# Performance work log

Measured on AMD Instinct MI355X. Metric: run time of the kernel, lower is better.

Reference implementation:

```python
import jax, jax.numpy as jnp
import numpy as np

N, V, D, H, E = 16384, 17, 128, 256, 32
LN_EPS = 1e-5


def setup_inputs() -> dict:
    key = jax.random.key(0)
    ks = jax.random.split(key, 16)
    s = lambda *sh: 1.0 / np.sqrt(sh[0])
    inp = {
        "h": jax.random.normal(ks[0], (N, V, D), dtype=jnp.float32),
        "xy": jax.random.normal(ks[1], (N, V, 2), dtype=jnp.float32),
        "joint_mask": jax.random.randint(ks[2], (N, V), 0, 2).astype(bool),
        "edge_index": jax.random.randint(ks[3], (E, 2), 0, V).astype(jnp.int64),
        # edge MLP: Linear(2D+2 -> H), ReLU, Linear(H -> D)
        "ew1": jax.random.normal(ks[4], (2 * D + 2, H), dtype=jnp.float32) * s(2 * D + 2),
        "eb1": jnp.zeros((H,), dtype=jnp.float32),
        "ew2": jax.random.normal(ks[5], (H, D), dtype=jnp.float32) * s(H),
        "eb2": jnp.zeros((D,), dtype=jnp.float32),
        # node MLP: Linear(2D -> H), ReLU, Linear(H -> D)
        "nw1": jax.random.normal(ks[6], (2 * D, H), dtype=jnp.float32) * s(2 * D),
        "nb1": jnp.zeros((H,), dtype=jnp.float32),
        "nw2": jax.random.normal(ks[7], (H, D), dtype=jnp.float32) * s(H),
        "nb2": jnp.zeros((D,), dtype=jnp.float32),
        # LayerNorm(D)
        "gamma": jnp.ones((D,), dtype=jnp.float32),
        "beta": jnp.zeros((D,), dtype=jnp.float32),
    }
    return inp


def reference(h, xy, joint_mask, edge_index, ew1, eb1, ew2, eb2,
              nw1, nb1, nw2, nb2, gamma, beta):
    dst = edge_index[:, 0]  # [E]
    src = edge_index[:, 1]  # [E]
    mask_f = joint_mask.astype(h.dtype)  # [N,V]

    target = h[:, dst, :]                  # [N,E,D]
    source = h[:, src, :]                  # [N,E,D]
    rel = xy[:, src, :] - xy[:, dst, :]    # [N,E,2]
    edge_valid = (joint_mask[:, dst] & joint_mask[:, src]).astype(h.dtype)  # [N,E]

    msg_in = jnp.concatenate([target, source, rel], axis=-1)  # [N,E,2D+2]
    msg = jax.nn.relu(msg_in @ ew1 + eb1) @ ew2 + eb2          # [N,E,D]
    msg = msg * edge_valid[..., None]

    agg = jnp.zeros_like(h).at[:, dst, :].add(msg)                           # [N,V,D]
    denom = jnp.zeros((h.shape[0], h.shape[1], 1), h.dtype).at[:, dst, :].add(
        edge_valid[..., None])                                               # [N,V,1]
    agg = agg / jnp.maximum(denom, 1.0)

    delta = jax.nn.relu(jnp.concatenate([h, agg], axis=-1) @ nw1 + nb1) @ nw2 + nb2
    has_neighbors = (denom > 0).astype(h.dtype)
    x = h + delta * has_neighbors

    mu = jnp.mean(x, axis=-1, keepdims=True)
    var = jnp.mean(jnp.square(x - mu), axis=-1, keepdims=True)
    out = (x - mu) / jnp.sqrt(var + LN_EPS) * gamma + beta
    return out * mask_f[..., None]
```

## Files before the change

kernel.cpp:

```cpp
#include <hip/hip_runtime.h>

typedef _Float16 half8 __attribute__((ext_vector_type(8)));
typedef _Float16 half4v __attribute__((ext_vector_type(4)));
typedef float f32x4 __attribute__((ext_vector_type(4)));
typedef unsigned int u32;

#define LDH 136

__global__ void prep_weights(const float* __restrict__ ew1,
                             const float* __restrict__ ew2,
                             const float* __restrict__ nw1,
                             const float* __restrict__ nw2,
                             _Float16* __restrict__ wz) {
  int o = blockIdx.x * 256 + threadIdx.x;
  if (o < 65536) {
    int s = o >> 12, r = o & 4095;
    int gs = r >> 9, lane = (r >> 3) & 63, j = r & 7;
    int k = ((s & 1) * 4 + (gs >> 1)) * 32 + (lane >> 4) * 8 + j;
    int n = (s >> 1) * 32 + (gs & 1) * 16 + (lane & 15);
    wz[o] = (_Float16)ew1[k * 256 + n];
  } else if (o < 98304) {
    int o2 = o - 65536;
    int nc = o2 >> 12, r = o2 & 4095;
    int nt2 = r >> 9, lane = (r >> 3) & 63, j = r & 7;
    int k = nc * 32 + (lane >> 4) * 8 + j;
    int n = nt2 * 16 + (lane & 15);
    wz[o] = (_Float16)ew2[k * 128 + n];
  } else if (o < 163840) {
    int o2 = o - 98304;
    int s = o2 >> 12, r = o2 & 4095;
    int gs = r >> 9, lane = (r >> 3) & 63, j = r & 7;
    int k = ((s & 1) * 4 + (gs >> 1)) * 32 + (lane >> 4) * 8 + j;
    int n = (s >> 1) * 32 + (gs & 1) * 16 + (lane & 15);
    wz[o] = (_Float16)nw1[k * 256 + n];
  } else if (o < 196608) {
    int o2 = o - 163840;
    int nc = o2 >> 12, r = o2 & 4095;
    int nt2 = r >> 9, lane = (r >> 3) & 63, j = r & 7;
    int k = nc * 32 + (lane >> 4) * 8 + j;
    int n = nt2 * 16 + (lane & 15);
    wz[o] = (_Float16)nw2[k * 128 + n];
  }
}

__global__ __launch_bounds__(256, 2)
void fused_graph_layer(const float* __restrict__ h, const float* __restrict__ xy,
                       const int* __restrict__ jmask, const int* __restrict__ eidx,
                       const float* __restrict__ ew1,
                       const float* __restrict__ eb1, const float* __restrict__ eb2,
                       const float* __restrict__ nb1, const float* __restrict__ nb2,
                       const float* __restrict__ gamma, const float* __restrict__ beta,
                       const _Float16* __restrict__ wz,
                       float* __restrict__ out) {
  __shared__ _Float16 sh_h16[68 * LDH];
  __shared__ _Float16 sh_agg16[68 * LDH];
  __shared__ char uni[36864] __attribute__((aligned(16)));
  __shared__ float sh_rel[256];
  __shared__ float sh_valid[128];
  __shared__ float sh_dn[80];
  __shared__ float sh_hasn[68], sh_maskf[68];
  __shared__ int   sh_edge[64];

  const int tid  = threadIdx.x;
  const int wave = tid >> 6;
  const int lane = tid & 63;
  const int ln   = lane & 15;
  const int quad = lane >> 4;
  const int n0   = blockIdx.x * 4;
  const size_t hbase = (size_t)n0 * 2176;
  const f32x4 vzero = {0.f, 0.f, 0.f, 0.f};

  _Float16* ws = (_Float16*)(uni + wave * 9216);

  const _Float16* w1img  = wz;
  const _Float16* w2img  = wz + 65536;
  const _Float16* nw1img = wz + 98304;
  const _Float16* nw2img = wz + 163840;
  const float* w1r0 = ew1 + 256 * 256;
  const float* w1r1 = ew1 + 257 * 256;

  if (tid < 64) sh_edge[tid] = eidx[tid];
  if (tid < 68) sh_maskf[tid] = (float)jmask[n0 * 17 + tid];
  for (int i = tid; i < 2176; i += 256) {
    const float4 hv = ((const float4*)(h + hbase))[i];
    int q = i << 2;
    int gv = q >> 7, d = q & 127;
    half4v hq = { (_Float16)hv.x, (_Float16)hv.y, (_Float16)hv.z, (_Float16)hv.w };
    *(half4v*)&sh_h16[gv * LDH + d] = hq;
  }
  __syncthreads();
  if (tid < 128) {
    int g = tid >> 5, e = tid & 31;
    int dv = sh_edge[2 * e], sv = sh_edge[2 * e + 1];
    const float* xyb = xy + (size_t)(n0 + g) * 34;
    sh_rel[2 * tid]     = xyb[2 * sv]     - xyb[2 * dv];
    sh_rel[2 * tid + 1] = xyb[2 * sv + 1] - xyb[2 * dv + 1];
    sh_valid[tid] = sh_maskf[g * 17 + dv] * sh_maskf[g * 17 + sv];
  }
  __syncthreads();

  if (lane < 17) {
    float den = 0.f;
    for (int e = 0; e < 32; ++e)
      den += (sh_edge[2 * e] == lane) ? sh_valid[wave * 32 + e] : 0.f;
    sh_dn[wave * 20 + lane] = den;
    sh_hasn[wave * 17 + lane] = den > 0.f ? 1.f : 0.f;
  }

  int baseT[2], baseS[2];
  #pragma unroll
  for (int mi = 0; mi < 2; ++mi) {
    int eL = mi * 16 + ln;
    baseT[mi] = (wave * 17 + sh_edge[2 * eL]) * LDH;
    baseS[mi] = (wave * 17 + sh_edge[2 * eL + 1]) * LDH;
  }
  half8 af[2][8];
  #pragma unroll
  for (int mi = 0; mi < 2; ++mi)
    #pragma unroll
    for (int ks = 0; ks < 8; ++ks)
      af[mi][ks] = (ks < 4)
          ? *(const half8*)&sh_h16[baseT[mi] + ks * 32 + quad * 8]
          : *(const half8*)&sh_h16[baseS[mi] + (ks - 4) * 32 + quad * 8];

  f32x4 acc2[2][8];
  #pragma unroll
  for (int i = 0; i < 2; ++i)
    #pragma unroll
    for (int j = 0; j < 8; ++j) acc2[i][j] = vzero;

  for (int nc = 0; nc < 8; ++nc) {
    half8 b2f[8];
    #pragma unroll
    for (int t = 0; t < 8; ++t)
      b2f[t] = *(const half8*)(w2img + nc * 4096 + t * 512 + lane * 8);
    float ebv[2], r0v[2], r1v[2];
    #pragma unroll
    for (int nt = 0; nt < 2; ++nt) {
      int J = nc * 32 + nt * 16 + ln;
      ebv[nt] = eb1[J]; r0v[nt] = w1r0[J]; r1v[nt] = w1r1[J];
    }
    f32x4 acc1[2][2];
    #pragma unroll
    for (int i = 0; i < 2; ++i) { acc1[i][0] = vzero; acc1[i][1] = vzero; }

    #pragma unroll
    for (int kc = 0; kc < 8; ++kc) {
      const _Float16* wb = w1img + (size_t)(nc * 2 + (kc >> 2)) * 4096
                                 + ((kc & 3) * 2) * 512 + lane * 8;
      half8 bf0 = *(const half8*)wb;
      half8 bf1 = *(const half8*)(wb + 512);
      #pragma unroll
      for (int mi = 0; mi < 2; ++mi) {
        acc1[mi][0] = __builtin_amdgcn_mfma_f32_16x16x32_f16(af[mi][kc], bf0, acc1[mi][0], 0, 0, 0);
        acc1[mi][1] = __builtin_amdgcn_mfma_f32_16x16x32_f16(af[mi][kc], bf1, acc1[mi][1], 0, 0, 0);
      }
    }
    #pragma unroll
    for (int nt = 0; nt < 2; ++nt)
      #pragma unroll
      for (int mi = 0; mi < 2; ++mi)
        #pragma unroll
        for (int r = 0; r < 4; ++r) {
          int R = wave * 32 + mi * 16 + quad * 4 + r;
          float2 rr = *(const float2*)&sh_rel[2 * R];
          float val = acc1[mi][nt][r] + ebv[nt] + rr.x * r0v[nt] + rr.y * r1v[nt];
          ws[(mi * 16 + quad * 4 + r) * 40 + nt * 16 + ln] = (_Float16)fmaxf(val, 0.f);
        }
    #pragma unroll
    for (int mi = 0; mi < 2; ++mi) {
      half8 a2 = *(const half8*)&ws[(mi * 16 + ln) * 40 + quad * 8];
      #pragma unroll
      for (int nt2 = 0; nt2 < 8; ++nt2)
        acc2[mi][nt2] = __builtin_amdgcn_mfma_f32_16x16x32_f16(a2, b2f[nt2], acc2[mi][nt2], 0, 0, 0);
    }
  }

  {
    float eb2v[8];
    #pragma unroll
    for (int t = 0; t < 8; ++t) eb2v[t] = eb2[t * 16 + ln];
    #pragma unroll
    for (int mi = 0; mi < 2; ++mi)
      #pragma unroll
      for (int nt2 = 0; nt2 < 8; ++nt2) {
        half4v pk;
        #pragma unroll
        for (int r = 0; r < 4; ++r)
          pk[r] = (_Float16)(acc2[mi][nt2][r] + eb2v[nt2]);
        *(half4v*)&ws[(nt2 * 16 + ln) * 36 + mi * 16 + quad * 4] = pk;
      }
    half8 s0, s1;
    #pragma unroll
    for (int j = 0; j < 8; ++j) {
      int k = quad * 8 + j;
      int dk = sh_edge[2 * k];
      _Float16 vk = (_Float16)sh_valid[wave * 32 + k];
      s0[j] = (dk == ln) ? vk : (_Float16)0.f;
      s1[j] = (ln == 0 && dk == 16) ? vk : (_Float16)0.f;
    }
    f32x4 agg0[8], agg1[8];
    #pragma unroll
    for (int nt2 = 0; nt2 < 8; ++nt2) {
      half8 bfr = *(const half8*)&ws[(nt2 * 16 + ln) * 36 + quad * 8];
      agg0[nt2] = __builtin_amdgcn_mfma_f32_16x16x32_f16(s0, bfr, vzero, 0, 0, 0);
      agg1[nt2] = __builtin_amdgcn_mfma_f32_16x16x32_f16(s1, bfr, vzero, 0, 0, 0);
    }
    float rden[4];
    #pragma unroll
    for (int r = 0; r < 4; ++r)
      rden[r] = 1.f / fmaxf(sh_dn[wave * 20 + quad * 4 + r], 1.f);
    float rden16 = 1.f / fmaxf(sh_dn[wave * 20 + 16], 1.f);
    #pragma unroll
    for (int nt2 = 0; nt2 < 8; ++nt2) {
      #pragma unroll
      for (int r = 0; r < 4; ++r)
        sh_agg16[(wave * 17 + quad * 4 + r) * LDH + nt2 * 16 + ln] =
            (_Float16)(agg0[nt2][r] * rden[r]);
      if (quad == 0)
        sh_agg16[(wave * 17 + 16) * LDH + nt2 * 16 + ln] =
            (_Float16)(agg1[nt2][0] * rden16);
    }
  }
  __syncthreads();

  const int Rn = wave * 16 + ln;
  half8 afn0[8];
  #pragma unroll
  for (int ks = 0; ks < 8; ++ks)
    afn0[ks] = (ks < 4)
        ? *(const half8*)&sh_h16[Rn * LDH + ks * 32 + quad * 8]
        : *(const half8*)&sh_agg16[Rn * LDH + (ks - 4) * 32 + quad * 8];
  half8 afn1[8];
  if (wave == 0) {
    const int Rx = (64 + ln < 68) ? 64 + ln : 67;
    #pragma unroll
    for (int ks = 0; ks < 8; ++ks)
      afn1[ks] = (ks < 4)
          ? *(const half8*)&sh_h16[Rx * LDH + ks * 32 + quad * 8]
          : *(const half8*)&sh_agg16[Rx * LDH + (ks - 4) * 32 + quad * 8];
  }

  f32x4 acc4a[8], acc4b[8];
  #pragma unroll
  for (int j = 0; j < 8; ++j) { acc4a[j] = vzero; acc4b[j] = vzero; }

  for (int nc = 0; nc < 8; ++nc) {
    half8 b2n[8];
    #pragma unroll
    for (int t = 0; t < 8; ++t)
      b2n[t] = *(const half8*)(nw2img + nc * 4096 + t * 512 + lane * 8);
    float nbv[2];
    #pragma unroll
    for (int nt = 0; nt < 2; ++nt) nbv[nt] = nb1[nc * 32 + nt * 16 + ln];

    f32x4 acc3a[2], acc3b[2];
    acc3a[0] = vzero; acc3a[1] = vzero; acc3b[0] = vzero; acc3b[1] = vzero;

    #pragma unroll
    for (int kc = 0; kc < 8; ++kc) {
      const _Float16* wb = nw1img + (size_t)(nc * 2 + (kc >> 2)) * 4096
                                  + ((kc & 3) * 2) * 512 + lane * 8;
      half8 bf0 = *(const half8*)wb;
      half8 bf1 = *(const half8*)(wb + 512);
      acc3a[0] = __builtin_amdgcn_mfma_f32_16x16x32_f16(afn0[kc], bf0, acc3a[0], 0, 0, 0);
      acc3a[1] = __builtin_amdgcn_mfma_f32_16x16x32_f16(afn0[kc], bf1, acc3a[1], 0, 0, 0);
      if (wave == 0) {
        acc3b[0] = __builtin_amdgcn_mfma_f32_16x16x32_f16(afn1[kc], bf0, acc3b[0], 0, 0, 0);
        acc3b[1] = __builtin_amdgcn_mfma_f32_16x16x32_f16(afn1[kc], bf1, acc3b[1], 0, 0, 0);
      }
    }
    #pragma unroll
    for (int nt = 0; nt < 2; ++nt)
      #pragma unroll
      for (int r = 0; r < 4; ++r)
        ws[(quad * 4 + r) * 40 + nt * 16 + ln] = (_Float16)fmaxf(acc3a[nt][r] + nbv[nt], 0.f);
    if (wave == 0) {
      #pragma unroll
      for (int nt = 0; nt < 2; ++nt)
        #pragma unroll
        for (int r = 0; r < 4; ++r)
          ws[(16 + quad * 4 + r) * 40 + nt * 16 + ln] = (_Float16)fmaxf(acc3b[nt][r] + nbv[nt], 0.f);
    }
    {
      half8 a2 = *(const half8*)&ws[ln * 40 + quad * 8];
      #pragma unroll
      for (int nt2 = 0; nt2 < 8; ++nt2)
        acc4a[nt2] = __builtin_amdgcn_mfma_f32_16x16x32_f16(a2, b2n[nt2], acc4a[nt2], 0, 0, 0);
    }
    if (wave == 0) {
      half8 a2b = *(const half8*)&ws[(16 + ln) * 40 + quad * 8];
      #pragma unroll
      for (int nt2 = 0; nt2 < 8; ++nt2)
        acc4b[nt2] = __builtin_amdgcn_mfma_f32_16x16x32_f16(a2b, b2n[nt2], acc4b[nt2], 0, 0, 0);
    }
  }

  float gam[8], bet[8], nb2v[8];
  #pragma unroll
  for (int nt2 = 0; nt2 < 8; ++nt2) {
    int d = nt2 * 16 + ln;
    gam[nt2] = gamma[d]; bet[nt2] = beta[d]; nb2v[nt2] = nb2[d];
  }
  __syncthreads();
  float* ost = (float*)uni;
  {
    float xv[8][4];
    #pragma unroll
    for (int nt2 = 0; nt2 < 8; ++nt2) {
      int d = nt2 * 16 + ln;
      #pragma unroll
      for (int r = 0; r < 4; ++r) {
        int R = wave * 16 + quad * 4 + r;
        xv[nt2][r] = (float)sh_h16[R * LDH + d] + (acc4a[nt2][r] + nb2v[nt2]) * sh_hasn[R];
      }
    }
    #pragma unroll
    for (int r = 0; r < 4; ++r) {
      float s = 0.f, s2 = 0.f;
      #pragma unroll
      for (int nt2 = 0; nt2 < 8; ++nt2) { float x = xv[nt2][r]; s += x; s2 += x * x; }
      #pragma unroll
      for (int m = 1; m < 16; m <<= 1) { s += __shfl_xor(s, m, 64); s2 += __shfl_xor(s2, m, 64); }
      float mu = s * (1.f / 128.f);
      float var = s2 * (1.f / 128.f) - mu * mu;
      float rstd = rsqrtf(var + 1e-5f);
      int R = wave * 16 + quad * 4 + r;
      float mk = sh_maskf[R];
      #pragma unroll
      for (int nt2 = 0; nt2 < 8; ++nt2) {
        int d = nt2 * 16 + ln;
        ost[R * 132 + d] = ((xv[nt2][r] - mu) * rstd * gam[nt2] + bet[nt2]) * mk;
      }
    }
  }
  if (wave == 0) {
    float xv[8][4];
    #pragma unroll
    for (int nt2 = 0; nt2 < 8; ++nt2) {
      int d = nt2 * 16 + ln;
      #pragma unroll
      for (int r = 0; r < 4; ++r) {
        int R = 64 + quad * 4 + r;
        int Rc = R < 68 ? R : 67;
        xv[nt2][r] = (float)sh_h16[Rc * LDH + d] + (acc4b[nt2][r] + nb2v[nt2]) * sh_hasn[Rc];
      }
    }
    #pragma unroll
    for (int r = 0; r < 4; ++r) {
      float s = 0.f, s2 = 0.f;
      #pragma unroll
      for (int nt2 = 0; nt2 < 8; ++nt2) { float x = xv[nt2][r]; s += x; s2 += x * x; }
      #pragma unroll
      for (int m = 1; m < 16; m <<= 1) { s += __shfl_xor(s, m, 64); s2 += __shfl_xor(s2, m, 64); }
      float mu = s * (1.f / 128.f);
      float var = s2 * (1.f / 128.f) - mu * mu;
      float rstd = rsqrtf(var + 1e-5f);
      int R = 64 + quad * 4 + r;
      if (R < 68) {
        float mk = sh_maskf[R];
        #pragma unroll
        for (int nt2 = 0; nt2 < 8; ++nt2) {
          int d = nt2 * 16 + ln;
          ost[R * 132 + d] = ((xv[nt2][r] - mu) * rstd * gam[nt2] + bet[nt2]) * mk;
        }
      }
    }
  }
  __syncthreads();
  for (int i = tid; i < 8704; i += 256)
    out[hbase + i] = ost[(i >> 7) * 132 + (i & 127)];
}

extern "C" void kernel_launch(void* const* d_in, const int* in_sizes, int n_in,
                              void* d_out, int out_size, void* d_ws, size_t ws_size,
                              hipStream_t stream) {
  const float* h     = (const float*)d_in[0];
  const float* xy    = (const float*)d_in[1];
  const int*   jm    = (const int*)d_in[2];
  const int*   ei    = (const int*)d_in[3];
  const float* ew1   = (const float*)d_in[4];
  const float* eb1   = (const float*)d_in[5];
  const float* ew2   = (const float*)d_in[6];
  const float* eb2   = (const float*)d_in[7];
  const float* nw1   = (const float*)d_in[8];
  const float* nb1   = (const float*)d_in[9];
  const float* nw2   = (const float*)d_in[10];
  const float* nb2   = (const float*)d_in[11];
  const float* gamma = (const float*)d_in[12];
  const float* beta  = (const float*)d_in[13];
  _Float16* wz = (_Float16*)d_ws;

  prep_weights<<<768, 256, 0, stream>>>(ew1, ew2, nw1, nw2, wz);
  fused_graph_layer<<<4096, 256, 0, stream>>>(h, xy, jm, ei, ew1, eb1, eb2,
                                              nb1, nb2, gamma, beta, wz,
                                              (float*)d_out);
}
```

Baseline: 632.3 us.

## Shrink per-wave LDS scratch and write output directly to raise occupancy

Replaces the large shared union buffer with a smaller per-wave scratch by staging the edge-message transpose two column tiles at a time. The aggregation MFMAs are interleaved with those chunks. The final LayerNorm results now go straight to global memory instead of through a shared staging tile, which drops two block barriers. Launch bounds rise to three blocks per CU, so more blocks can be resident, at the cost of tighter register limits and less coalesced 64-byte-strided output stores.

```diff
diff --git a/kernel.cpp b/kernel.cpp
--- a/kernel.cpp
+++ b/kernel.cpp
@@ -43,7 +43,7 @@
   }
 }
 
-__global__ __launch_bounds__(256, 2)
+__global__ __launch_bounds__(256, 3)
 void fused_graph_layer(const float* __restrict__ h, const float* __restrict__ xy,
                        const int* __restrict__ jmask, const int* __restrict__ eidx,
                        const float* __restrict__ ew1,
@@ -54,7 +54,7 @@
                        float* __restrict__ out) {
   __shared__ _Float16 sh_h16[68 * LDH];
   __shared__ _Float16 sh_agg16[68 * LDH];
-  __shared__ char uni[36864] __attribute__((aligned(16)));
+  __shared__ _Float16 sh_ws[4 * 1280];
   __shared__ float sh_rel[256];
   __shared__ float sh_valid[128];
   __shared__ float sh_dn[80];
@@ -70,7 +70,7 @@
   const size_t hbase = (size_t)n0 * 2176;
   const f32x4 vzero = {0.f, 0.f, 0.f, 0.f};
 
-  _Float16* ws = (_Float16*)(uni + wave * 9216);
+  _Float16* ws = sh_ws + wave * 1280;
 
   const _Float16* w1img  = wz;
   const _Float16* w2img  = wz + 65536;
@@ -180,16 +180,6 @@
     float eb2v[8];
     #pragma unroll
     for (int t = 0; t < 8; ++t) eb2v[t] = eb2[t * 16 + ln];
-    #pragma unroll
-    for (int mi = 0; mi < 2; ++mi)
-      #pragma unroll
-      for (int nt2 = 0; nt2 < 8; ++nt2) {
-        half4v pk;
-        #pragma unroll
-        for (int r = 0; r < 4; ++r)
-          pk[r] = (_Float16)(acc2[mi][nt2][r] + eb2v[nt2]);
-        *(half4v*)&ws[(nt2 * 16 + ln) * 36 + mi * 16 + quad * 4] = pk;
-      }
     half8 s0, s1;
     #pragma unroll
     for (int j = 0; j < 8; ++j) {
@@ -199,27 +189,40 @@
       s0[j] = (dk == ln) ? vk : (_Float16)0.f;
       s1[j] = (ln == 0 && dk == 16) ? vk : (_Float16)0.f;
     }
-    f32x4 agg0[8], agg1[8];
-    #pragma unroll
-    for (int nt2 = 0; nt2 < 8; ++nt2) {
-      half8 bfr = *(const half8*)&ws[(nt2 * 16 + ln) * 36 + quad * 8];
-      agg0[nt2] = __builtin_amdgcn_mfma_f32_16x16x32_f16(s0, bfr, vzero, 0, 0, 0);
-      agg1[nt2] = __builtin_amdgcn_mfma_f32_16x16x32_f16(s1, bfr, vzero, 0, 0, 0);
-    }
     float rden[4];
     #pragma unroll
     for (int r = 0; r < 4; ++r)
       rden[r] = 1.f / fmaxf(sh_dn[wave * 20 + quad * 4 + r], 1.f);
     float rden16 = 1.f / fmaxf(sh_dn[wave * 20 + 16], 1.f);
-    #pragma unroll
-    for (int nt2 = 0; nt2 < 8; ++nt2) {
-      #pragma unroll
-      for (int r = 0; r < 4; ++r)
-        sh_agg16[(wave * 17 + quad * 4 + r) * LDH + nt2 * 16 + ln] =
-            (_Float16)(agg0[nt2][r] * rden[r]);
-      if (quad == 0)
-        sh_agg16[(wave * 17 + 16) * LDH + nt2 * 16 + ln] =
-            (_Float16)(agg1[nt2][0] * rden16);
+
+    #pragma unroll
+    for (int qh = 0; qh < 4; ++qh) {
+      #pragma unroll
+      for (int t = 0; t < 2; ++t) {
+        int nt2 = qh * 2 + t;
+        #pragma unroll
+        for (int mi = 0; mi < 2; ++mi) {
+          half4v pk;
+          #pragma unroll
+          for (int r = 0; r < 4; ++r)
+            pk[r] = (_Float16)(acc2[mi][nt2][r] + eb2v[nt2]);
+          *(half4v*)&ws[(t * 16 + ln) * 40 + mi * 16 + quad * 4] = pk;
+        }
+      }
+      #pragma unroll
+      for (int t = 0; t < 2; ++t) {
+        int nt2 = qh * 2 + t;
+        half8 bfr = *(const half8*)&ws[(t * 16 + ln) * 40 + quad * 8];
+        f32x4 agg0 = __builtin_amdgcn_mfma_f32_16x16x32_f16(s0, bfr, vzero, 0, 0, 0);
+        f32x4 agg1 = __builtin_amdgcn_mfma_f32_16x16x32_f16(s1, bfr, vzero, 0, 0, 0);
+        #pragma unroll
+        for (int r = 0; r < 4; ++r)
+          sh_agg16[(wave * 17 + quad * 4 + r) * LDH + nt2 * 16 + ln] =
+              (_Float16)(agg0[r] * rden[r]);
+        if (quad == 0)
+          sh_agg16[(wave * 17 + 16) * LDH + nt2 * 16 + ln] =
+              (_Float16)(agg1[0] * rden16);
+      }
     }
   }
   __syncthreads();
@@ -302,8 +305,6 @@
     int d = nt2 * 16 + ln;
     gam[nt2] = gamma[d]; bet[nt2] = beta[d]; nb2v[nt2] = nb2[d];
   }
-  __syncthreads();
-  float* ost = (float*)uni;
   {
     float xv[8][4];
     #pragma unroll
@@ -327,11 +328,10 @@
       float rstd = rsqrtf(var + 1e-5f);
       int R = wave * 16 + quad * 4 + r;
       float mk = sh_maskf[R];
-      #pragma unroll
-      for (int nt2 = 0; nt2 < 8; ++nt2) {
-        int d = nt2 * 16 + ln;
-        ost[R * 132 + d] = ((xv[nt2][r] - mu) * rstd * gam[nt2] + bet[nt2]) * mk;
-      }
+      float* orow = out + hbase + (size_t)R * 128 + ln;
+      #pragma unroll
+      for (int nt2 = 0; nt2 < 8; ++nt2)
+        orow[nt2 * 16] = ((xv[nt2][r] - mu) * rstd * gam[nt2] + bet[nt2]) * mk;
     }
   }
   if (wave == 0) {
@@ -359,17 +359,13 @@
       int R = 64 + quad * 4 + r;
       if (R < 68) {
         float mk = sh_maskf[R];
-        #pragma unroll
-        for (int nt2 = 0; nt2 < 8; ++nt2) {
-          int d = nt2 * 16 + ln;
-          ost[R * 132 + d] = ((xv[nt2][r] - mu) * rstd * gam[nt2] + bet[nt2]) * mk;
-        }
-      }
-    }
-  }
-  __syncthreads();
-  for (int i = tid; i < 8704; i += 256)
-    out[hbase + i] = ost[(i >> 7) * 132 + (i & 127)];
+        float* orow = out + hbase + (size_t)R * 128 + ln;
+        #pragma unroll
+        for (int nt2 = 0; nt2 < 8; ++nt2)
+          orow[nt2 * 16] = ((xv[nt2][r] - mu) * rstd * gam[nt2] + bet[nt2]) * mk;
+      }
+    }
+  }
 }
 
 extern "C" void kernel_launch(void* const* d_in, const int* in_sizes, int n_in,
```

New measurement: 776.5 us. 1.23x slower.
